# Optimization experiments

Measured on AMD Instinct MI355X. Metric: run time of the kernel, lower is better.

## Reference

```python
import jax, jax.numpy as jnp
import numpy as np

NUM_USERS = 1_000_000
NUM_ITEMS = 100_000
EMB = 128
IN_DIM = 2 * EMB
E = 8          # num_experts
H = 256        # expert_hidden
T = 2          # num_tasks
TH = 128       # tower_hidden
B = 16384


def setup_inputs() -> dict:
    key = jax.random.key(0)
    ks = jax.random.split(key, 16)
    s = lambda fan_in: 1.0 / np.sqrt(fan_in)
    return {
        "user_idx": jax.random.randint(ks[0], (B,), 0, NUM_USERS),
        "item_idx": jax.random.randint(ks[1], (B,), 0, NUM_ITEMS),
        "user_table": jax.random.normal(ks[2], (NUM_USERS, EMB), jnp.float32),
        "item_table": jax.random.normal(ks[3], (NUM_ITEMS, EMB), jnp.float32),
        "eW1": jax.random.normal(ks[4], (E, IN_DIM, H), jnp.float32) * s(IN_DIM),
        "eb1": jnp.zeros((E, H), jnp.float32),
        "eW2": jax.random.normal(ks[5], (E, H, H), jnp.float32) * s(H),
        "eb2": jnp.zeros((E, H), jnp.float32),
        "gW": jax.random.normal(ks[6], (T, IN_DIM, E), jnp.float32) * s(IN_DIM),
        "gb": jnp.zeros((T, E), jnp.float32),
        "tW1": jax.random.normal(ks[7], (T, H, TH), jnp.float32) * s(H),
        "tb1": jnp.zeros((T, TH), jnp.float32),
        "tW2": jax.random.normal(ks[8], (T, TH, 1), jnp.float32) * s(TH),
        "tb2": jnp.zeros((T, 1), jnp.float32),
    }


def reference(user_idx, item_idx, user_table, item_table,
              eW1, eb1, eW2, eb2, gW, gb, tW1, tb1, tW2, tb2):
    # Embedding lookup + concat: [B, 2*EMB]
    x = jnp.concatenate([user_table[user_idx], item_table[item_idx]], axis=1)
    # All experts batched: [B, E, H]
    h1 = jax.nn.relu(jnp.einsum('bi,eih->beh', x, eW1) + eb1[None])
    expert_out = jax.nn.relu(jnp.einsum('beh,ehk->bek', h1, eW2) + eb2[None])
    # Gates: [T, B, E] softmax over experts
    gate_w = jax.nn.softmax(jnp.einsum('bi,tie->tbe', x, gW) + gb[:, None, :], axis=-1)
    # Weighted combine: [T, B, H]
    mmoe = jnp.einsum('beh,tbe->tbh', expert_out, gate_w)
    # Towers: [T, B]
    th = jax.nn.relu(jnp.einsum('tbh,thk->tbk', mmoe, tW1) + tb1[:, None, :])
    out = (jnp.einsum('tbk,tko->tbo', th, tW2) + tb2[:, None, :]).squeeze(-1)
    return out  # [T, B] (torch returns list of T [B] tensors)
```

## Files before the change

### kernel.cpp

```cpp
#include <hip/hip_runtime.h>
#include <hip/hip_bf16.h>

typedef __bf16 bf16x8 __attribute__((ext_vector_type(8)));
typedef float f32x4 __attribute__((ext_vector_type(4)));

#define NB 16384
#define NE 8

__device__ __forceinline__ unsigned short f2bf(float f) {
  unsigned u = __float_as_uint(f);
  u += 0x7fff + ((u >> 16) & 1);
  return (unsigned short)(u >> 16);
}
__device__ __forceinline__ float bf2f(unsigned short s) {
  return __uint_as_float(((unsigned)s) << 16);
}
__device__ __forceinline__ void async16(const void* g, void* lds) {
  __builtin_amdgcn_global_load_lds(
      (const __attribute__((address_space(1))) unsigned int*)g,
      (__attribute__((address_space(3))) unsigned int*)lds, 16, 0, 0);
}

__global__ void gather_kernel(const int* __restrict__ uidx,
                              const int* __restrict__ iidx,
                              const float* __restrict__ ut,
                              const float* __restrict__ it,
                              unsigned short* __restrict__ xbf) {
  int s = blockIdx.x * 4 + (threadIdx.x >> 6);
  int lane = threadIdx.x & 63;
  const float* src = (lane < 32)
      ? ut + (size_t)uidx[s] * 128 + lane * 4
      : it + (size_t)iidx[s] * 128 + (lane - 32) * 4;
  float4 v = *(const float4*)src;
  ushort4 bv;
  bv.x = f2bf(v.x); bv.y = f2bf(v.y); bv.z = f2bf(v.z); bv.w = f2bf(v.w);
  *(ushort4*)(xbf + s * 256 + lane * 4) = bv;
}

__global__ void prep_kernel(const float* __restrict__ eW1, const float* __restrict__ eW2,
                            const float* __restrict__ tW1, const float* __restrict__ gW,
                            unsigned short* __restrict__ w1t, unsigned short* __restrict__ w2t,
                            unsigned short* __restrict__ tw1t, unsigned short* __restrict__ gwt2) {
  int blk = blockIdx.x;
  int tid = threadIdx.x;
  if (blk == 272) {
    int k = tid;
#pragma unroll
    for (int t = 0; t < 2; ++t)
#pragma unroll
      for (int e = 0; e < 8; ++e)
        gwt2[(t * 8 + e) * 256 + k] = f2bf(gW[(t * 256 + k) * 8 + e]);
    return;
  }
  __shared__ float T[64][68];
  const float* src; unsigned short* dst; int src_ld;
  if (blk < 128) {
    int e = blk >> 4, kt = (blk >> 2) & 3, nt = blk & 3;
    src = eW1 + ((size_t)e * 256 + kt * 64) * 256 + nt * 64;
    dst = w1t + ((size_t)e * 256 + nt * 64) * 256 + kt * 64;
    src_ld = 256;
  } else if (blk < 256) {
    int b2 = blk - 128;
    int e = b2 >> 4, kt = (b2 >> 2) & 3, nt = b2 & 3;
    src = eW2 + ((size_t)e * 256 + kt * 64) * 256 + nt * 64;
    dst = w2t + ((size_t)e * 256 + nt * 64) * 256 + kt * 64;
    src_ld = 256;
  } else {
    int b2 = blk - 256;
    int t = b2 >> 3, kt = (b2 >> 1) & 3, nt = b2 & 1;
    src = tW1 + ((size_t)t * 256 + kt * 64) * 128 + nt * 64;
    dst = tw1t + ((size_t)t * 128 + nt * 64) * 256 + kt * 64;
    src_ld = 128;
  }
  int rg = tid >> 4, cg = tid & 15;
#pragma unroll
  for (int i = 0; i < 4; ++i) {
    int row = rg + i * 16, col = cg * 4;
    float4 v = *(const float4*)(src + row * src_ld + col);
    T[row][col] = v.x; T[row][col + 1] = v.y; T[row][col + 2] = v.z; T[row][col + 3] = v.w;
  }
  __syncthreads();
#pragma unroll
  for (int i = 0; i < 4; ++i) {
    int n = rg + i * 16, k4 = cg * 4;
    ushort4 o;
    o.x = f2bf(T[k4 + 0][n]); o.y = f2bf(T[k4 + 1][n]);
    o.z = f2bf(T[k4 + 2][n]); o.w = f2bf(T[k4 + 3][n]);
    *(ushort4*)(dst + n * 256 + k4) = o;
  }
}

__global__ void gate_kernel(const unsigned short* __restrict__ xbf,
                            const unsigned short* __restrict__ gwt2,
                            const float* __restrict__ gb,
                            float* __restrict__ gates) {
  int tid = threadIdx.x, lane = tid & 63, w = tid >> 6;
  int m = lane & 15, q = lane >> 4;
  int brow = blockIdx.x * 64 + w * 16;
  const unsigned short* xp = xbf + (brow + m) * 256 + q * 8;
  const unsigned short* gp = gwt2 + m * 256 + q * 8;
  f32x4 acc = {0.f, 0.f, 0.f, 0.f};
#pragma unroll
  for (int ks = 0; ks < 8; ++ks) {
    bf16x8 a = *(const bf16x8*)(xp + ks * 32);
    bf16x8 b = *(const bf16x8*)(gp + ks * 32);
    acc = __builtin_amdgcn_mfma_f32_16x16x32_bf16(a, b, acc, 0, 0, 0);
  }
  float bias = gb[m];
#pragma unroll
  for (int r = 0; r < 4; ++r) {
    float lg = acc[r] + bias;
    float mx = lg;
#pragma unroll
    for (int d = 1; d < 8; d <<= 1) mx = fmaxf(mx, __shfl_xor(mx, d));
    float ev = __expf(lg - mx);
    float sm = ev;
#pragma unroll
    for (int d = 1; d < 8; d <<= 1) sm += __shfl_xor(sm, d);
    int b = brow + q * 4 + r;
    gates[(((m >> 3) << 14) + b) * 8 + (m & 7)] = ev / sm;
  }
}

__global__ __launch_bounds__(256, 2) void expert_kernel(
    const unsigned short* __restrict__ xbf, const unsigned short* __restrict__ w1t,
    const unsigned short* __restrict__ w2t, const float* __restrict__ eb1,
    const float* __restrict__ eb2, unsigned short* __restrict__ eo) {
  __shared__ unsigned short Xs[64 * 256];
  __shared__ unsigned short H1[64 * 256];
  const int b0 = blockIdx.x * 64;
  const int e = blockIdx.y;
  const int tid = threadIdx.x, lane = tid & 63, w = tid >> 6;
  const int m = lane & 15, q = lane >> 4;

#pragma unroll
  for (int is = 0; is < 8; ++is) {
    int C = is * 256 + tid;
    int row = C >> 5, p = C & 31;
    int l = (p & ~7) | ((p ^ row) & 7);
    async16(xbf + (b0 + row) * 256 + l * 8,
            (char*)Xs + (is * 256 + w * 64) * 16);
  }
  __syncthreads();

  f32x4 acc[4][4];
  f32x4 z4 = {0.f, 0.f, 0.f, 0.f};
#pragma unroll
  for (int ct = 0; ct < 4; ++ct)
#pragma unroll
    for (int rt = 0; rt < 4; ++rt) acc[ct][rt] = z4;

  const unsigned short* wp1 = w1t + ((size_t)(e * 256 + w * 64 + m)) * 256 + q * 8;
#pragma unroll 2
  for (int ks = 0; ks < 8; ++ks) {
    bf16x8 aw[4], bx[4];
#pragma unroll
    for (int ct = 0; ct < 4; ++ct)
      aw[ct] = *(const bf16x8*)(wp1 + ct * 16 * 256 + ks * 32);
#pragma unroll
    for (int rt = 0; rt < 4; ++rt) {
      int bl = rt * 16 + m;
      int c = ks * 4 + q;
      int p = (c & ~7) | ((c ^ bl) & 7);
      bx[rt] = *(const bf16x8*)(Xs + bl * 256 + p * 8);
    }
#pragma unroll
    for (int ct = 0; ct < 4; ++ct)
#pragma unroll
      for (int rt = 0; rt < 4; ++rt)
        acc[ct][rt] = __builtin_amdgcn_mfma_f32_16x16x32_bf16(aw[ct], bx[rt], acc[ct][rt], 0, 0, 0);
  }
#pragma unroll
  for (int ct = 0; ct < 4; ++ct) {
    int n4 = w * 64 + ct * 16 + q * 4;
    float4 bias = *(const float4*)(eb1 + e * 256 + n4);
    int c = n4 >> 3;
#pragma unroll
    for (int rt = 0; rt < 4; ++rt) {
      int bl = rt * 16 + m;
      int p = (c & ~7) | ((c ^ bl) & 7);
      ushort4 hv;
      hv.x = f2bf(fmaxf(acc[ct][rt][0] + bias.x, 0.f));
      hv.y = f2bf(fmaxf(acc[ct][rt][1] + bias.y, 0.f));
      hv.z = f2bf(fmaxf(acc[ct][rt][2] + bias.z, 0.f));
      hv.w = f2bf(fmaxf(acc[ct][rt][3] + bias.w, 0.f));
      *(ushort4*)(H1 + bl * 256 + p * 8 + (q & 1) * 4) = hv;
    }
  }
#pragma unroll
  for (int ct = 0; ct < 4; ++ct)
#pragma unroll
    for (int rt = 0; rt < 4; ++rt) acc[ct][rt] = z4;
  __syncthreads();

  const unsigned short* wp2 = w2t + ((size_t)(e * 256 + w * 64 + m)) * 256 + q * 8;
#pragma unroll 2
  for (int ks = 0; ks < 8; ++ks) {
    bf16x8 aw[4], bh[4];
#pragma unroll
    for (int ct = 0; ct < 4; ++ct)
      aw[ct] = *(const bf16x8*)(wp2 + ct * 16 * 256 + ks * 32);
#pragma unroll
    for (int rt = 0; rt < 4; ++rt) {
      int bl = rt * 16 + m;
      int c = ks * 4 + q;
      int p = (c & ~7) | ((c ^ bl) & 7);
      bh[rt] = *(const bf16x8*)(H1 + bl * 256 + p * 8);
    }
#pragma unroll
    for (int ct = 0; ct < 4; ++ct)
#pragma unroll
      for (int rt = 0; rt < 4; ++rt)
        acc[ct][rt] = __builtin_amdgcn_mfma_f32_16x16x32_bf16(aw[ct], bh[rt], acc[ct][rt], 0, 0, 0);
  }
#pragma unroll
  for (int ct = 0; ct < 4; ++ct) {
    int n4 = w * 64 + ct * 16 + q * 4;
    float4 bias = *(const float4*)(eb2 + e * 256 + n4);
#pragma unroll
    for (int rt = 0; rt < 4; ++rt) {
      int b = b0 + rt * 16 + m;
      ushort4 ov;
      ov.x = f2bf(fmaxf(acc[ct][rt][0] + bias.x, 0.f));
      ov.y = f2bf(fmaxf(acc[ct][rt][1] + bias.y, 0.f));
      ov.z = f2bf(fmaxf(acc[ct][rt][2] + bias.z, 0.f));
      ov.w = f2bf(fmaxf(acc[ct][rt][3] + bias.w, 0.f));
      *(ushort4*)(eo + ((size_t)b * 8 + e) * 256 + n4) = ov;
    }
  }
}

__global__ __launch_bounds__(256, 2) void tower_kernel(
    const unsigned short* __restrict__ eo, const float* __restrict__ gates,
    const unsigned short* __restrict__ tw1t, const float* __restrict__ tb1,
    const float* __restrict__ tW2, const float* __restrict__ tb2,
    float* __restrict__ out) {
  __shared__ unsigned short MM[64 * 264];
  const int b0 = blockIdx.x * 64;
  const int t = blockIdx.y;
  const int tid = threadIdx.x, lane = tid & 63, w = tid >> 6;
  const int m = lane & 15, q = lane >> 4;

  {
    int bl = tid >> 2, hq = tid & 3;
    float g[8];
#pragma unroll
    for (int e = 0; e < 8; ++e) g[e] = gates[((t << 14) + b0 + bl) * 8 + e];
    const unsigned short* ep = eo + (size_t)(b0 + bl) * 8 * 256;
#pragma unroll
    for (int ch = 0; ch < 4; ++ch) {
      int h0 = hq * 64 + ch * 16;
      float a16[16];
#pragma unroll
      for (int j = 0; j < 16; ++j) a16[j] = 0.f;
#pragma unroll
      for (int e = 0; e < 8; ++e) {
#pragma unroll
        for (int j = 0; j < 4; ++j) {
          ushort4 v = *(const ushort4*)(ep + e * 256 + h0 + j * 4);
          a16[j * 4 + 0] += g[e] * bf2f(v.x);
          a16[j * 4 + 1] += g[e] * bf2f(v.y);
          a16[j * 4 + 2] += g[e] * bf2f(v.z);
          a16[j * 4 + 3] += g[e] * bf2f(v.w);
        }
      }
#pragma unroll
      for (int j = 0; j < 4; ++j) {
        ushort4 o;
        o.x = f2bf(a16[j * 4 + 0]); o.y = f2bf(a16[j * 4 + 1]);
        o.z = f2bf(a16[j * 4 + 2]); o.w = f2bf(a16[j * 4 + 3]);
        *(ushort4*)(MM + bl * 264 + h0 + j * 4) = o;
      }
    }
  }
  __syncthreads();

  const unsigned short* wp = tw1t + ((size_t)(t * 128 + m)) * 256 + q * 8;
  const unsigned short* mp = MM + (w * 16 + m) * 264 + q * 8;
  f32x4 acc[8];
  f32x4 z4 = {0.f, 0.f, 0.f, 0.f};
#pragma unroll
  for (int ct = 0; ct < 8; ++ct) acc[ct] = z4;
#pragma unroll 2
  for (int ks = 0; ks < 8; ++ks) {
    bf16x8 bm = *(const bf16x8*)(mp + ks * 32);
#pragma unroll
    for (int ct = 0; ct < 8; ++ct) {
      bf16x8 aw = *(const bf16x8*)(wp + ct * 16 * 256 + ks * 32);
      acc[ct] = __builtin_amdgcn_mfma_f32_16x16x32_bf16(aw, bm, acc[ct], 0, 0, 0);
    }
  }
  float s = 0.f;
#pragma unroll
  for (int ct = 0; ct < 8; ++ct) {
    int n4 = ct * 16 + q * 4;
    float4 b1 = *(const float4*)(tb1 + t * 128 + n4);
    float4 w2 = *(const float4*)(tW2 + t * 128 + n4);
    s += fmaxf(acc[ct][0] + b1.x, 0.f) * w2.x;
    s += fmaxf(acc[ct][1] + b1.y, 0.f) * w2.y;
    s += fmaxf(acc[ct][2] + b1.z, 0.f) * w2.z;
    s += fmaxf(acc[ct][3] + b1.w, 0.f) * w2.w;
  }
  s += __shfl_xor(s, 16);
  s += __shfl_xor(s, 32);
  if (lane < 16) out[(t << 14) + b0 + w * 16 + lane] = s + tb2[t];
}

extern "C" void kernel_launch(void* const* d_in, const int* in_sizes, int n_in,
                              void* d_out, int out_size, void* d_ws, size_t ws_size,
                              hipStream_t stream) {
  (void)in_sizes; (void)n_in; (void)out_size; (void)ws_size;
  const int*   uidx = (const int*)d_in[0];
  const int*   iidx = (const int*)d_in[1];
  const float* ut   = (const float*)d_in[2];
  const float* it   = (const float*)d_in[3];
  const float* eW1  = (const float*)d_in[4];
  const float* eb1  = (const float*)d_in[5];
  const float* eW2  = (const float*)d_in[6];
  const float* eb2  = (const float*)d_in[7];
  const float* gW   = (const float*)d_in[8];
  const float* gb   = (const float*)d_in[9];
  const float* tW1  = (const float*)d_in[10];
  const float* tb1  = (const float*)d_in[11];
  const float* tW2  = (const float*)d_in[12];
  const float* tb2  = (const float*)d_in[13];
  float* out = (float*)d_out;

  char* p = (char*)d_ws;
  unsigned short* xbf  = (unsigned short*)p; p += (size_t)NB * 256 * 2;
  unsigned short* w1t  = (unsigned short*)p; p += (size_t)NE * 256 * 256 * 2;
  unsigned short* w2t  = (unsigned short*)p; p += (size_t)NE * 256 * 256 * 2;
  unsigned short* tw1t = (unsigned short*)p; p += (size_t)2 * 128 * 256 * 2;
  unsigned short* gwt2 = (unsigned short*)p; p += (size_t)16 * 256 * 2;
  float* gates         = (float*)p;          p += (size_t)2 * NB * 8 * 4;
  unsigned short* eo   = (unsigned short*)p; p += (size_t)NB * NE * 256 * 2;

  gather_kernel<<<NB / 4, 256, 0, stream>>>(uidx, iidx, ut, it, xbf);
  prep_kernel<<<273, 256, 0, stream>>>(eW1, eW2, tW1, gW, w1t, w2t, tw1t, gwt2);
  gate_kernel<<<NB / 64, 256, 0, stream>>>(xbf, gwt2, gb, gates);
  expert_kernel<<<dim3(NB / 64, NE), 256, 0, stream>>>(xbf, w1t, w2t, eb1, eb2, eo);
  tower_kernel<<<dim3(NB / 64, 2), 256, 0, stream>>>(eo, gates, tw1t, tb1, tW2, tb2, out);
}
```

Measured before the change: 777.5 us.

## Fuse experts, gated combine and towers into one kernel with MFMA-fragment weight layout

Replaces the separate expert and tower kernels with one kernel per 64-row batch tile that loops over all 8 experts. It accumulates the gate-weighted expert outputs in registers and then runs both towers from LDS. This removes the large bf16 expert-output round trip through global memory (16384x8x256). Weights are pre-packed in MFMA fragment order so each lane does one contiguous 16-byte load, and gates are interleaved per row. The trade-off is only 256 blocks of 512 threads, so the grid covers the device once with less parallelism, plus extra syncs inside the expert loop.

After: 677.7 us. 12.8% less time.

```diff
diff --git a/kernel.cpp b/kernel.cpp
--- a/kernel.cpp
+++ b/kernel.cpp
@@ -5,15 +5,11 @@
 typedef float f32x4 __attribute__((ext_vector_type(4)));
 
 #define NB 16384
-#define NE 8
 
 __device__ __forceinline__ unsigned short f2bf(float f) {
   unsigned u = __float_as_uint(f);
   u += 0x7fff + ((u >> 16) & 1);
   return (unsigned short)(u >> 16);
-}
-__device__ __forceinline__ float bf2f(unsigned short s) {
-  return __uint_as_float(((unsigned)s) << 16);
 }
 __device__ __forceinline__ void async16(const void* g, void* lds) {
   __builtin_amdgcn_global_load_lds(
@@ -39,71 +35,62 @@
 
 __global__ void prep_kernel(const float* __restrict__ eW1, const float* __restrict__ eW2,
                             const float* __restrict__ tW1, const float* __restrict__ gW,
-                            unsigned short* __restrict__ w1t, unsigned short* __restrict__ w2t,
-                            unsigned short* __restrict__ tw1t, unsigned short* __restrict__ gwt2) {
-  int blk = blockIdx.x;
-  int tid = threadIdx.x;
-  if (blk == 272) {
-    int k = tid;
-#pragma unroll
-    for (int t = 0; t < 2; ++t)
-#pragma unroll
-      for (int e = 0; e < 8; ++e)
-        gwt2[(t * 8 + e) * 256 + k] = f2bf(gW[(t * 256 + k) * 8 + e]);
-    return;
-  }
-  __shared__ float T[64][68];
-  const float* src; unsigned short* dst; int src_ld;
+                            unsigned short* __restrict__ w1f, unsigned short* __restrict__ w2f,
+                            unsigned short* __restrict__ twf, unsigned short* __restrict__ gwf) {
+  int blk = blockIdx.x, tid = threadIdx.x;
+  int m = tid & 15, q = (tid >> 4) & 3, g3 = tid >> 6;
   if (blk < 128) {
-    int e = blk >> 4, kt = (blk >> 2) & 3, nt = blk & 3;
-    src = eW1 + ((size_t)e * 256 + kt * 64) * 256 + nt * 64;
-    dst = w1t + ((size_t)e * 256 + nt * 64) * 256 + kt * 64;
-    src_ld = 256;
-  } else if (blk < 256) {
-    int b2 = blk - 128;
-    int e = b2 >> 4, kt = (b2 >> 2) & 3, nt = b2 & 3;
-    src = eW2 + ((size_t)e * 256 + kt * 64) * 256 + nt * 64;
-    dst = w2t + ((size_t)e * 256 + nt * 64) * 256 + kt * 64;
-    src_ld = 256;
+    int l = blk >> 6;
+    int r = blk & 63;
+    int e = r >> 3, ks = r & 7;
+    const float* src = (l ? eW2 : eW1) + (size_t)e * 65536;
+    unsigned short* dst = l ? w2f : w1f;
+#pragma unroll
+    for (int i = 0; i < 4; ++i) {
+      int nt = i * 4 + g3;
+      unsigned short o[8];
+#pragma unroll
+      for (int j = 0; j < 8; ++j)
+        o[j] = f2bf(src[(ks * 32 + q * 8 + j) * 256 + nt * 16 + m]);
+      *(uint4*)(dst + (size_t)((e * 16 + nt) * 8 + ks) * 512 + (q * 16 + m) * 8) = *(uint4*)o;
+    }
+  } else if (blk < 144) {
+    int idx = blk - 128;
+    int t = idx >> 3, ks = idx & 7;
+#pragma unroll
+    for (int i = 0; i < 2; ++i) {
+      int nt = i * 4 + g3;
+      unsigned short o[8];
+#pragma unroll
+      for (int j = 0; j < 8; ++j)
+        o[j] = f2bf(tW1[((size_t)t * 256 + ks * 32 + q * 8 + j) * 128 + nt * 16 + m]);
+      *(uint4*)(twf + (size_t)((t * 8 + nt) * 8 + ks) * 512 + (q * 16 + m) * 8) = *(uint4*)o;
+    }
   } else {
-    int b2 = blk - 256;
-    int t = b2 >> 3, kt = (b2 >> 1) & 3, nt = b2 & 1;
-    src = tW1 + ((size_t)t * 256 + kt * 64) * 128 + nt * 64;
-    dst = tw1t + ((size_t)t * 128 + nt * 64) * 256 + kt * 64;
-    src_ld = 128;
-  }
-  int rg = tid >> 4, cg = tid & 15;
-#pragma unroll
-  for (int i = 0; i < 4; ++i) {
-    int row = rg + i * 16, col = cg * 4;
-    float4 v = *(const float4*)(src + row * src_ld + col);
-    T[row][col] = v.x; T[row][col + 1] = v.y; T[row][col + 2] = v.z; T[row][col + 3] = v.w;
-  }
-  __syncthreads();
-#pragma unroll
-  for (int i = 0; i < 4; ++i) {
-    int n = rg + i * 16, k4 = cg * 4;
-    ushort4 o;
-    o.x = f2bf(T[k4 + 0][n]); o.y = f2bf(T[k4 + 1][n]);
-    o.z = f2bf(T[k4 + 2][n]); o.w = f2bf(T[k4 + 3][n]);
-    *(ushort4*)(dst + n * 256 + k4) = o;
+    int ks = blk - 144;
+    if (tid < 64) {
+      unsigned short o[8];
+#pragma unroll
+      for (int j = 0; j < 8; ++j)
+        o[j] = f2bf(gW[((m >> 3) * 256 + ks * 32 + q * 8 + j) * 8 + (m & 7)]);
+      *(uint4*)(gwf + ks * 512 + tid * 8) = *(uint4*)o;
+    }
   }
 }
 
 __global__ void gate_kernel(const unsigned short* __restrict__ xbf,
-                            const unsigned short* __restrict__ gwt2,
+                            const unsigned short* __restrict__ gwf,
                             const float* __restrict__ gb,
-                            float* __restrict__ gates) {
+                            float* __restrict__ gbuf) {
   int tid = threadIdx.x, lane = tid & 63, w = tid >> 6;
   int m = lane & 15, q = lane >> 4;
   int brow = blockIdx.x * 64 + w * 16;
   const unsigned short* xp = xbf + (brow + m) * 256 + q * 8;
-  const unsigned short* gp = gwt2 + m * 256 + q * 8;
   f32x4 acc = {0.f, 0.f, 0.f, 0.f};
 #pragma unroll
   for (int ks = 0; ks < 8; ++ks) {
     bf16x8 a = *(const bf16x8*)(xp + ks * 32);
-    bf16x8 b = *(const bf16x8*)(gp + ks * 32);
+    bf16x8 b = *(const bf16x8*)(gwf + ks * 512 + lane * 8);
     acc = __builtin_amdgcn_mfma_f32_16x16x32_bf16(a, b, acc, 0, 0, 0);
   }
   float bias = gb[m];
@@ -118,192 +105,183 @@
 #pragma unroll
     for (int d = 1; d < 8; d <<= 1) sm += __shfl_xor(sm, d);
     int b = brow + q * 4 + r;
-    gates[(((m >> 3) << 14) + b) * 8 + (m & 7)] = ev / sm;
-  }
-}
-
-__global__ __launch_bounds__(256, 2) void expert_kernel(
-    const unsigned short* __restrict__ xbf, const unsigned short* __restrict__ w1t,
-    const unsigned short* __restrict__ w2t, const float* __restrict__ eb1,
-    const float* __restrict__ eb2, unsigned short* __restrict__ eo) {
-  __shared__ unsigned short Xs[64 * 256];
-  __shared__ unsigned short H1[64 * 256];
+    gbuf[b * 16 + (m & 7) * 2 + (m >> 3)] = ev / sm;
+  }
+}
+
+__global__ __launch_bounds__(512, 2) void mega_kernel(
+    const unsigned short* __restrict__ xbf, const unsigned short* __restrict__ w1f,
+    const unsigned short* __restrict__ w2f, const float* __restrict__ eb1,
+    const float* __restrict__ eb2, const float* __restrict__ gbuf,
+    const unsigned short* __restrict__ twf, const float* __restrict__ tb1,
+    const float* __restrict__ tW2, const float* __restrict__ tb2,
+    float* __restrict__ out) {
+  __shared__ unsigned short smem[32768];
+  unsigned short* Xs = smem;
+  unsigned short* H1 = smem + 16384;
   const int b0 = blockIdx.x * 64;
-  const int e = blockIdx.y;
   const int tid = threadIdx.x, lane = tid & 63, w = tid >> 6;
   const int m = lane & 15, q = lane >> 4;
 
 #pragma unroll
-  for (int is = 0; is < 8; ++is) {
-    int C = is * 256 + tid;
+  for (int is = 0; is < 4; ++is) {
+    int C = is * 512 + tid;
     int row = C >> 5, p = C & 31;
     int l = (p & ~7) | ((p ^ row) & 7);
-    async16(xbf + (b0 + row) * 256 + l * 8,
-            (char*)Xs + (is * 256 + w * 64) * 16);
+    async16(xbf + (b0 + row) * 256 + l * 8, (char*)Xs + is * 8192 + w * 1024);
   }
   __syncthreads();
 
-  f32x4 acc[4][4];
   f32x4 z4 = {0.f, 0.f, 0.f, 0.f};
-#pragma unroll
-  for (int ct = 0; ct < 4; ++ct)
-#pragma unroll
-    for (int rt = 0; rt < 4; ++rt) acc[ct][rt] = z4;
-
-  const unsigned short* wp1 = w1t + ((size_t)(e * 256 + w * 64 + m)) * 256 + q * 8;
-#pragma unroll 2
-  for (int ks = 0; ks < 8; ++ks) {
-    bf16x8 aw[4], bx[4];
-#pragma unroll
-    for (int ct = 0; ct < 4; ++ct)
-      aw[ct] = *(const bf16x8*)(wp1 + ct * 16 * 256 + ks * 32);
-#pragma unroll
-    for (int rt = 0; rt < 4; ++rt) {
-      int bl = rt * 16 + m;
+  f32x4 macc[2][2][4];
+#pragma unroll
+  for (int t = 0; t < 2; ++t)
+#pragma unroll
+    for (int ct = 0; ct < 2; ++ct)
+#pragma unroll
+      for (int rt = 0; rt < 4; ++rt) macc[t][ct][rt] = z4;
+
+  for (int e = 0; e < 8; ++e) {
+    f32x4 acc[2][4];
+#pragma unroll
+    for (int ct = 0; ct < 2; ++ct)
+#pragma unroll
+      for (int rt = 0; rt < 4; ++rt) acc[ct][rt] = z4;
+
+    const unsigned short* wp1 = w1f + (size_t)((e * 16 + w * 2) * 8) * 512 + lane * 8;
+#pragma unroll
+    for (int ks = 0; ks < 8; ++ks) {
+      bf16x8 aw0 = *(const bf16x8*)(wp1 + ks * 512);
+      bf16x8 aw1 = *(const bf16x8*)(wp1 + (ks + 8) * 512);
       int c = ks * 4 + q;
+#pragma unroll
+      for (int rt = 0; rt < 4; ++rt) {
+        int bl = rt * 16 + m;
+        int p = (c & ~7) | ((c ^ bl) & 7);
+        bf16x8 bx = *(const bf16x8*)(Xs + bl * 256 + p * 8);
+        acc[0][rt] = __builtin_amdgcn_mfma_f32_16x16x32_bf16(aw0, bx, acc[0][rt], 0, 0, 0);
+        acc[1][rt] = __builtin_amdgcn_mfma_f32_16x16x32_bf16(aw1, bx, acc[1][rt], 0, 0, 0);
+      }
+    }
+    __syncthreads();
+#pragma unroll
+    for (int ct = 0; ct < 2; ++ct) {
+      int n4 = w * 32 + ct * 16 + q * 4;
+      float4 b1 = *(const float4*)(eb1 + e * 256 + n4);
+      int c = n4 >> 3;
+#pragma unroll
+      for (int rt = 0; rt < 4; ++rt) {
+        int bl = rt * 16 + m;
+        int p = (c & ~7) | ((c ^ bl) & 7);
+        ushort4 hv;
+        hv.x = f2bf(fmaxf(acc[ct][rt][0] + b1.x, 0.f));
+        hv.y = f2bf(fmaxf(acc[ct][rt][1] + b1.y, 0.f));
+        hv.z = f2bf(fmaxf(acc[ct][rt][2] + b1.z, 0.f));
+        hv.w = f2bf(fmaxf(acc[ct][rt][3] + b1.w, 0.f));
+        *(ushort4*)(H1 + bl * 256 + p * 8 + (q & 1) * 4) = hv;
+      }
+    }
+    __syncthreads();
+    float2 g2[4];
+#pragma unroll
+    for (int rt = 0; rt < 4; ++rt)
+      g2[rt] = *(const float2*)(gbuf + (b0 + rt * 16 + m) * 16 + e * 2);
+
+#pragma unroll
+    for (int ct = 0; ct < 2; ++ct)
+#pragma unroll
+      for (int rt = 0; rt < 4; ++rt) acc[ct][rt] = z4;
+    const unsigned short* wp2 = w2f + (size_t)((e * 16 + w * 2) * 8) * 512 + lane * 8;
+#pragma unroll
+    for (int ks = 0; ks < 8; ++ks) {
+      bf16x8 aw0 = *(const bf16x8*)(wp2 + ks * 512);
+      bf16x8 aw1 = *(const bf16x8*)(wp2 + (ks + 8) * 512);
+      int c = ks * 4 + q;
+#pragma unroll
+      for (int rt = 0; rt < 4; ++rt) {
+        int bl = rt * 16 + m;
+        int p = (c & ~7) | ((c ^ bl) & 7);
+        bf16x8 bh = *(const bf16x8*)(H1 + bl * 256 + p * 8);
+        acc[0][rt] = __builtin_amdgcn_mfma_f32_16x16x32_bf16(aw0, bh, acc[0][rt], 0, 0, 0);
+        acc[1][rt] = __builtin_amdgcn_mfma_f32_16x16x32_bf16(aw1, bh, acc[1][rt], 0, 0, 0);
+      }
+    }
+#pragma unroll
+    for (int ct = 0; ct < 2; ++ct) {
+      int n4 = w * 32 + ct * 16 + q * 4;
+      float4 b2 = *(const float4*)(eb2 + e * 256 + n4);
+#pragma unroll
+      for (int rt = 0; rt < 4; ++rt) {
+        float g0 = g2[rt].x, g1 = g2[rt].y;
+        float eo0 = fmaxf(acc[ct][rt][0] + b2.x, 0.f);
+        float eo1 = fmaxf(acc[ct][rt][1] + b2.y, 0.f);
+        float eo2 = fmaxf(acc[ct][rt][2] + b2.z, 0.f);
+        float eo3 = fmaxf(acc[ct][rt][3] + b2.w, 0.f);
+        macc[0][ct][rt][0] += g0 * eo0; macc[1][ct][rt][0] += g1 * eo0;
+        macc[0][ct][rt][1] += g0 * eo1; macc[1][ct][rt][1] += g1 * eo1;
+        macc[0][ct][rt][2] += g0 * eo2; macc[1][ct][rt][2] += g1 * eo2;
+        macc[0][ct][rt][3] += g0 * eo3; macc[1][ct][rt][3] += g1 * eo3;
+      }
+    }
+  }
+  __syncthreads();
+
+#pragma unroll
+  for (int t = 0; t < 2; ++t) {
+    unsigned short* MMt = smem + t * 16384;
+#pragma unroll
+    for (int ct = 0; ct < 2; ++ct) {
+      int n4 = w * 32 + ct * 16 + q * 4;
+      int c = n4 >> 3;
+#pragma unroll
+      for (int rt = 0; rt < 4; ++rt) {
+        int bl = rt * 16 + m;
+        int p = (c & ~7) | ((c ^ bl) & 7);
+        ushort4 mv;
+        mv.x = f2bf(macc[t][ct][rt][0]);
+        mv.y = f2bf(macc[t][ct][rt][1]);
+        mv.z = f2bf(macc[t][ct][rt][2]);
+        mv.w = f2bf(macc[t][ct][rt][3]);
+        *(ushort4*)(MMt + bl * 256 + p * 8 + (q & 1) * 4) = mv;
+      }
+    }
+  }
+  __syncthreads();
+
+  {
+    int t = w >> 2, brow = (w & 3) * 16;
+    const unsigned short* MMt = smem + t * 16384;
+    const unsigned short* wp = twf + (size_t)(t * 64) * 512 + lane * 8;
+    f32x4 at[8];
+#pragma unroll
+    for (int ct = 0; ct < 8; ++ct) at[ct] = z4;
+#pragma unroll
+    for (int ks = 0; ks < 8; ++ks) {
+      int c = ks * 4 + q;
+      int bl = brow + m;
       int p = (c & ~7) | ((c ^ bl) & 7);
-      bx[rt] = *(const bf16x8*)(Xs + bl * 256 + p * 8);
-    }
-#pragma unroll
-    for (int ct = 0; ct < 4; ++ct)
-#pragma unroll
-      for (int rt = 0; rt < 4; ++rt)
-        acc[ct][rt] = __builtin_amdgcn_mfma_f32_16x16x32_bf16(aw[ct], bx[rt], acc[ct][rt], 0, 0, 0);
-  }
-#pragma unroll
-  for (int ct = 0; ct < 4; ++ct) {
-    int n4 = w * 64 + ct * 16 + q * 4;
-    float4 bias = *(const float4*)(eb1 + e * 256 + n4);
-    int c = n4 >> 3;
-#pragma unroll
-    for (int rt = 0; rt < 4; ++rt) {
-      int bl = rt * 16 + m;
-      int p = (c & ~7) | ((c ^ bl) & 7);
-      ushort4 hv;
-      hv.x = f2bf(fmaxf(acc[ct][rt][0] + bias.x, 0.f));
-      hv.y = f2bf(fmaxf(acc[ct][rt][1] + bias.y, 0.f));
-      hv.z = f2bf(fmaxf(acc[ct][rt][2] + bias.z, 0.f));
-      hv.w = f2bf(fmaxf(acc[ct][rt][3] + bias.w, 0.f));
-      *(ushort4*)(H1 + bl * 256 + p * 8 + (q & 1) * 4) = hv;
-    }
-  }
-#pragma unroll
-  for (int ct = 0; ct < 4; ++ct)
-#pragma unroll
-    for (int rt = 0; rt < 4; ++rt) acc[ct][rt] = z4;
-  __syncthreads();
-
-  const unsigned short* wp2 = w2t + ((size_t)(e * 256 + w * 64 + m)) * 256 + q * 8;
-#pragma unroll 2
-  for (int ks = 0; ks < 8; ++ks) {
-    bf16x8 aw[4], bh[4];
-#pragma unroll
-    for (int ct = 0; ct < 4; ++ct)
-      aw[ct] = *(const bf16x8*)(wp2 + ct * 16 * 256 + ks * 32);
-#pragma unroll
-    for (int rt = 0; rt < 4; ++rt) {
-      int bl = rt * 16 + m;
-      int c = ks * 4 + q;
-      int p = (c & ~7) | ((c ^ bl) & 7);
-      bh[rt] = *(const bf16x8*)(H1 + bl * 256 + p * 8);
-    }
-#pragma unroll
-    for (int ct = 0; ct < 4; ++ct)
-#pragma unroll
-      for (int rt = 0; rt < 4; ++rt)
-        acc[ct][rt] = __builtin_amdgcn_mfma_f32_16x16x32_bf16(aw[ct], bh[rt], acc[ct][rt], 0, 0, 0);
-  }
-#pragma unroll
-  for (int ct = 0; ct < 4; ++ct) {
-    int n4 = w * 64 + ct * 16 + q * 4;
-    float4 bias = *(const float4*)(eb2 + e * 256 + n4);
-#pragma unroll
-    for (int rt = 0; rt < 4; ++rt) {
-      int b = b0 + rt * 16 + m;
-      ushort4 ov;
-      ov.x = f2bf(fmaxf(acc[ct][rt][0] + bias.x, 0.f));
-      ov.y = f2bf(fmaxf(acc[ct][rt][1] + bias.y, 0.f));
-      ov.z = f2bf(fmaxf(acc[ct][rt][2] + bias.z, 0.f));
-      ov.w = f2bf(fmaxf(acc[ct][rt][3] + bias.w, 0.f));
-      *(ushort4*)(eo + ((size_t)b * 8 + e) * 256 + n4) = ov;
-    }
-  }
-}
-
-__global__ __launch_bounds__(256, 2) void tower_kernel(
-    const unsigned short* __restrict__ eo, const float* __restrict__ gates,
-    const unsigned short* __restrict__ tw1t, const float* __restrict__ tb1,
-    const float* __restrict__ tW2, const float* __restrict__ tb2,
-    float* __restrict__ out) {
-  __shared__ unsigned short MM[64 * 264];
-  const int b0 = blockIdx.x * 64;
-  const int t = blockIdx.y;
-  const int tid = threadIdx.x, lane = tid & 63, w = tid >> 6;
-  const int m = lane & 15, q = lane >> 4;
-
-  {
-    int bl = tid >> 2, hq = tid & 3;
-    float g[8];
-#pragma unroll
-    for (int e = 0; e < 8; ++e) g[e] = gates[((t << 14) + b0 + bl) * 8 + e];
-    const unsigned short* ep = eo + (size_t)(b0 + bl) * 8 * 256;
-#pragma unroll
-    for (int ch = 0; ch < 4; ++ch) {
-      int h0 = hq * 64 + ch * 16;
-      float a16[16];
-#pragma unroll
-      for (int j = 0; j < 16; ++j) a16[j] = 0.f;
-#pragma unroll
-      for (int e = 0; e < 8; ++e) {
-#pragma unroll
-        for (int j = 0; j < 4; ++j) {
-          ushort4 v = *(const ushort4*)(ep + e * 256 + h0 + j * 4);
-          a16[j * 4 + 0] += g[e] * bf2f(v.x);
-          a16[j * 4 + 1] += g[e] * bf2f(v.y);
-          a16[j * 4 + 2] += g[e] * bf2f(v.z);
-          a16[j * 4 + 3] += g[e] * bf2f(v.w);
-        }
-      }
-#pragma unroll
-      for (int j = 0; j < 4; ++j) {
-        ushort4 o;
-        o.x = f2bf(a16[j * 4 + 0]); o.y = f2bf(a16[j * 4 + 1]);
-        o.z = f2bf(a16[j * 4 + 2]); o.w = f2bf(a16[j * 4 + 3]);
-        *(ushort4*)(MM + bl * 264 + h0 + j * 4) = o;
-      }
-    }
-  }
-  __syncthreads();
-
-  const unsigned short* wp = tw1t + ((size_t)(t * 128 + m)) * 256 + q * 8;
-  const unsigned short* mp = MM + (w * 16 + m) * 264 + q * 8;
-  f32x4 acc[8];
-  f32x4 z4 = {0.f, 0.f, 0.f, 0.f};
-#pragma unroll
-  for (int ct = 0; ct < 8; ++ct) acc[ct] = z4;
-#pragma unroll 2
-  for (int ks = 0; ks < 8; ++ks) {
-    bf16x8 bm = *(const bf16x8*)(mp + ks * 32);
+      bf16x8 bm = *(const bf16x8*)(MMt + bl * 256 + p * 8);
+#pragma unroll
+      for (int ct = 0; ct < 8; ++ct) {
+        bf16x8 aw = *(const bf16x8*)(wp + (ct * 8 + ks) * 512);
+        at[ct] = __builtin_amdgcn_mfma_f32_16x16x32_bf16(aw, bm, at[ct], 0, 0, 0);
+      }
+    }
+    float s = 0.f;
 #pragma unroll
     for (int ct = 0; ct < 8; ++ct) {
-      bf16x8 aw = *(const bf16x8*)(wp + ct * 16 * 256 + ks * 32);
-      acc[ct] = __builtin_amdgcn_mfma_f32_16x16x32_bf16(aw, bm, acc[ct], 0, 0, 0);
-    }
-  }
-  float s = 0.f;
-#pragma unroll
-  for (int ct = 0; ct < 8; ++ct) {
-    int n4 = ct * 16 + q * 4;
-    float4 b1 = *(const float4*)(tb1 + t * 128 + n4);
-    float4 w2 = *(const float4*)(tW2 + t * 128 + n4);
-    s += fmaxf(acc[ct][0] + b1.x, 0.f) * w2.x;
-    s += fmaxf(acc[ct][1] + b1.y, 0.f) * w2.y;
-    s += fmaxf(acc[ct][2] + b1.z, 0.f) * w2.z;
-    s += fmaxf(acc[ct][3] + b1.w, 0.f) * w2.w;
-  }
-  s += __shfl_xor(s, 16);
-  s += __shfl_xor(s, 32);
-  if (lane < 16) out[(t << 14) + b0 + w * 16 + lane] = s + tb2[t];
+      int n4 = ct * 16 + q * 4;
+      float4 b1 = *(const float4*)(tb1 + t * 128 + n4);
+      float4 w2 = *(const float4*)(tW2 + t * 128 + n4);
+      s += fmaxf(at[ct][0] + b1.x, 0.f) * w2.x;
+      s += fmaxf(at[ct][1] + b1.y, 0.f) * w2.y;
+      s += fmaxf(at[ct][2] + b1.z, 0.f) * w2.z;
+      s += fmaxf(at[ct][3] + b1.w, 0.f) * w2.w;
+    }
+    s += __shfl_xor(s, 16);
+    s += __shfl_xor(s, 32);
+    if (lane < 16) out[(t << 14) + b0 + brow + lane] = s + tb2[t];
+  }
 }
 
 extern "C" void kernel_launch(void* const* d_in, const int* in_sizes, int n_in,
@@ -327,17 +305,16 @@
   float* out = (float*)d_out;
 
   char* p = (char*)d_ws;
-  unsigned short* xbf  = (unsigned short*)p; p += (size_t)NB * 256 * 2;
-  unsigned short* w1t  = (unsigned short*)p; p += (size_t)NE * 256 * 256 * 2;
-  unsigned short* w2t  = (unsigned short*)p; p += (size_t)NE * 256 * 256 * 2;
-  unsigned short* tw1t = (unsigned short*)p; p += (size_t)2 * 128 * 256 * 2;
-  unsigned short* gwt2 = (unsigned short*)p; p += (size_t)16 * 256 * 2;
-  float* gates         = (float*)p;          p += (size_t)2 * NB * 8 * 4;
-  unsigned short* eo   = (unsigned short*)p; p += (size_t)NB * NE * 256 * 2;
+  unsigned short* xbf = (unsigned short*)p; p += (size_t)NB * 256 * 2;
+  unsigned short* w1f = (unsigned short*)p; p += (size_t)8 * 16 * 8 * 512 * 2;
+  unsigned short* w2f = (unsigned short*)p; p += (size_t)8 * 16 * 8 * 512 * 2;
+  unsigned short* twf = (unsigned short*)p; p += (size_t)2 * 8 * 8 * 512 * 2;
+  unsigned short* gwf = (unsigned short*)p; p += (size_t)8 * 512 * 2;
+  float* gbuf         = (float*)p;          p += (size_t)NB * 16 * 4;
 
   gather_kernel<<<NB / 4, 256, 0, stream>>>(uidx, iidx, ut, it, xbf);
-  prep_kernel<<<273, 256, 0, stream>>>(eW1, eW2, tW1, gW, w1t, w2t, tw1t, gwt2);
-  gate_kernel<<<NB / 64, 256, 0, stream>>>(xbf, gwt2, gb, gates);
-  expert_kernel<<<dim3(NB / 64, NE), 256, 0, stream>>>(xbf, w1t, w2t, eb1, eb2, eo);
-  tower_kernel<<<dim3(NB / 64, 2), 256, 0, stream>>>(eo, gates, tw1t, tb1, tW2, tb2, out);
-}
+  prep_kernel<<<152, 256, 0, stream>>>(eW1, eW2, tW1, gW, w1f, w2f, twf, gwf);
+  gate_kernel<<<NB / 64, 256, 0, stream>>>(xbf, gwf, gb, gbuf);
+  mega_kernel<<<256, 512, 0, stream>>>(xbf, w1f, w2f, eb1, eb2, gbuf,
+                                       twf, tb1, tW2, tb2, out);
+}
```
